# Kernel optimization log

Hardware: AMD Instinct MI355X
Metric: run time of the kernel (lower is better)

## Reference

```python
import jax, jax.numpy as jnp
import numpy as np

M_MARGIN = 0.5
SCALE = 64.0
COS_M = float(np.cos(M_MARGIN))
SIN_M = float(np.sin(M_MARGIN))
TH = -COS_M
MM = SIN_M * M_MARGIN
NUM_CLASSES = 100000
IN_FEATURES = 512
BATCH = 512


def setup_inputs() -> dict:
    key = jax.random.key(0)
    k1, k2, k3 = jax.random.split(key, 3)
    x = jax.random.normal(k1, (BATCH, IN_FEATURES), dtype=jnp.float32)
    y = jax.random.randint(k2, (BATCH,), 0, NUM_CLASSES, dtype=jnp.int64 if jax.config.jax_enable_x64 else jnp.int32)
    # xavier_uniform-like init for weight [num_classes, in_features]
    limit = float(np.sqrt(6.0 / (NUM_CLASSES + IN_FEATURES)))
    weight = jax.random.uniform(k3, (NUM_CLASSES, IN_FEATURES), minval=-limit, maxval=limit, dtype=jnp.float32)
    return {"x": x, "y": y, "weight": weight}


def _l2_normalize(v, axis=-1, eps=1e-12):
    # matches F.normalize(p=2): v / max(||v||, eps)
    n = jnp.sqrt(jnp.sum(v * v, axis=axis, keepdims=True))
    return v / jnp.maximum(n, eps)


def reference(x, y, weight):
    # cosine logits: [B, C]
    xn = _l2_normalize(x)
    wn = _l2_normalize(weight)
    cos = jnp.einsum('bd,cd->bc', xn, wn)
    sin = jnp.sqrt(jnp.clip(1.0 - cos * cos, 0.0))
    cos_w_margin = cos * COS_M - sin * SIN_M
    cos_w_margin = jnp.where(cos > TH, cos_w_margin, cos - MM)
    ohe = jax.nn.one_hot(y, NUM_CLASSES, dtype=jnp.bool_)
    logit = jnp.where(ohe, cos_w_margin, cos) * SCALE
    # cross entropy, mean reduction
    logp = jax.nn.log_softmax(logit, axis=-1)
    nll = -jnp.take_along_axis(logp, y[:, None], axis=-1)[:, 0]
    return jnp.mean(nll)
```

## Files before the change

kernel.cpp:

```cpp
#include <hip/hip_runtime.h>
#include <hip/hip_bf16.h>
#include <cstdint>
#include <cstddef>

#define C_CLS   100000
#define D_FEAT  512
#define B_ROWS  512
#define NBN     782
#define NBLK    (4 * NBN)

#define COSM 0.8775825618903728f
#define SINM 0.479425538604203f
#define TH_  (-0.8775825618903728f)
#define MM_  0.2397127693021015f

typedef __bf16 bf16x8 __attribute__((ext_vector_type(8)));
typedef float  f32x4  __attribute__((ext_vector_type(4)));

typedef __attribute__((address_space(3))) void lds_void;
typedef const __attribute__((address_space(1))) void g_void;

__device__ __forceinline__ void async_copy16(const void* g, void* l) {
    __builtin_amdgcn_global_load_lds((g_void*)g, (lds_void*)l, 16, 0, 0);
}

__global__ void k_norm(const float* __restrict__ x, const float* __restrict__ w,
                       __bf16* __restrict__ xn, __bf16* __restrict__ wn,
                       float* __restrict__ row_sum, int* __restrict__ counter) {
    const int r4   = blockIdx.x * 4 + (threadIdx.x >> 6);
    const int lane = threadIdx.x & 63;
    const float* src;
    __bf16*      dst;
    if (r4 < C_CLS) {
        src = w  + (size_t)r4 * D_FEAT;
        dst = wn + (size_t)r4 * D_FEAT;
    } else {
        src = x  + (size_t)(r4 - C_CLS) * D_FEAT;
        dst = xn + (size_t)(r4 - C_CLS) * D_FEAT;
    }
    const f32x4* p = (const f32x4*)src;
    f32x4 a = p[lane * 2];
    f32x4 b = p[lane * 2 + 1];
    float s = a[0]*a[0] + a[1]*a[1] + a[2]*a[2] + a[3]*a[3]
            + b[0]*b[0] + b[1]*b[1] + b[2]*b[2] + b[3]*b[3];
    #pragma unroll
    for (int m = 32; m >= 1; m >>= 1) s += __shfl_xor(s, m, 64);
    const float inv = 1.0f / fmaxf(sqrtf(s), 1e-12f);
    bf16x8 o;
    o[0] = (__bf16)(a[0]*inv); o[1] = (__bf16)(a[1]*inv);
    o[2] = (__bf16)(a[2]*inv); o[3] = (__bf16)(a[3]*inv);
    o[4] = (__bf16)(b[0]*inv); o[5] = (__bf16)(b[1]*inv);
    o[6] = (__bf16)(b[2]*inv); o[7] = (__bf16)(b[3]*inv);
    *(bf16x8*)(dst + lane * 8) = o;

    if (blockIdx.x == C_CLS / 4) {
        row_sum[threadIdx.x]       = 0.0f;
        row_sum[threadIdx.x + 256] = 0.0f;
        if (threadIdx.x == 0) *counter = 0;
    }
}

__global__ __launch_bounds__(256, 4) void k_gemm(
        const __bf16* __restrict__ xn, const __bf16* __restrict__ wn,
        const int* __restrict__ y,
        float* __restrict__ row_sum, float* __restrict__ tlogit,
        int* __restrict__ counter, float* __restrict__ out) {

    __shared__ __align__(16) __bf16 As[2][4096];
    __shared__ __align__(16) __bf16 Bs[2][4096];
    __shared__ int   ys[128];
    __shared__ float red[2][128];
    __shared__ int   lastflag;
    __shared__ float pr[4];

    const int tid = threadIdx.x;
    const int wg = (blockIdx.x & 7) * (NBLK / 8) + (blockIdx.x >> 3);
    const int bm = wg & 3;
    const int bn = wg >> 2;

    if (tid < 128) ys[tid] = y[bm * 128 + tid];

    const int wave = tid >> 6;
    const int lane = tid & 63;
    const int wm   = wave >> 1;
    const int wn_  = wave & 1;
    const int quad = lane >> 4;
    const int l15  = lane & 15;

    f32x4 acc[4][4];
    #pragma unroll
    for (int i = 0; i < 4; ++i)
        #pragma unroll
        for (int j = 0; j < 4; ++j) acc[i][j] = (f32x4){0.f, 0.f, 0.f, 0.f};

    #define STAGE(s, kt_) do {                                                          \
        const int k0_ = (kt_) * 32;                                                     \
        _Pragma("unroll")                                                               \
        for (int i_ = 0; i_ < 2; ++i_) {                                                \
            const int c_ = tid + i_ * 256;                                              \
            const int qc_ = c_ >> 7, rc_ = c_ & 127;                                    \
            async_copy16(xn + (size_t)(bm * 128 + rc_) * D_FEAT + k0_ + qc_ * 8,        \
                         &As[s][c_ * 8]);                                               \
        }                                                                               \
        _Pragma("unroll")                                                               \
        for (int i_ = 0; i_ < 2; ++i_) {                                                \
            const int c_ = tid + i_ * 256;                                              \
            const int qc_ = c_ >> 7, rc_ = c_ & 127;                                    \
            int grow_ = bn * 128 + rc_; if (grow_ > C_CLS - 1) grow_ = C_CLS - 1;       \
            async_copy16(wn + (size_t)grow_ * D_FEAT + k0_ + qc_ * 8,                   \
                         &Bs[s][c_ * 8]);                                               \
        }                                                                               \
    } while (0)

    STAGE(0, 0);
    STAGE(1, 1);

    #pragma unroll
    for (int kt = 0; kt < 16; ++kt) {
        const int cur = kt & 1;

        if (kt < 15) asm volatile("s_waitcnt vmcnt(4)" ::: "memory");
        else         asm volatile("s_waitcnt vmcnt(0)" ::: "memory");
        __builtin_amdgcn_s_barrier();

        bf16x8 af[4];
        #pragma unroll
        for (int mi = 0; mi < 4; ++mi)
            af[mi] = *(const bf16x8*)&As[cur][(quad * 128 + wm * 64 + mi * 16 + l15) * 8];
        bf16x8 bfr[4];
        #pragma unroll
        for (int ni = 0; ni < 4; ++ni)
            bfr[ni] = *(const bf16x8*)&Bs[cur][(quad * 128 + wn_ * 64 + ni * 16 + l15) * 8];

        asm volatile("s_waitcnt lgkmcnt(0)" ::: "memory");
        __builtin_amdgcn_s_barrier();
        if (kt < 14) STAGE(cur, kt + 2);

        #pragma unroll
        for (int mi = 0; mi < 4; ++mi)
            #pragma unroll
            for (int ni = 0; ni < 4; ++ni)
                acc[mi][ni] = __builtin_amdgcn_mfma_f32_16x16x32_bf16(af[mi], bfr[ni], acc[mi][ni], 0, 0, 0);
    }
    #undef STAGE

    #pragma unroll
    for (int mi = 0; mi < 4; ++mi) {
        float rs[4] = {0.f, 0.f, 0.f, 0.f};
        #pragma unroll
        for (int ni = 0; ni < 4; ++ni) {
            const int gcol = bn * 128 + wn_ * 64 + ni * 16 + l15;
            const bool colv = (gcol < C_CLS);
            #pragma unroll
            for (int reg = 0; reg < 4; ++reg) {
                const int lrow = wm * 64 + mi * 16 + quad * 4 + reg;
                const float cosv = acc[mi][ni][reg];
                const float sinv = sqrtf(fmaxf(1.0f - cosv * cosv, 0.0f));
                const float phi  = (cosv > TH_) ? (cosv * COSM - sinv * SINM) : (cosv - MM_);
                const bool ist   = colv && (gcol == ys[lrow]);
                const float logit = 64.0f * (ist ? phi : cosv);
                if (ist) atomicExch(&tlogit[bm * 128 + lrow], logit);
                rs[reg] += colv ? __expf(logit - 64.0f) : 0.0f;
            }
        }
        #pragma unroll
        for (int reg = 0; reg < 4; ++reg) {
            float v = rs[reg];
            v += __shfl_xor(v, 8, 64);
            v += __shfl_xor(v, 4, 64);
            v += __shfl_xor(v, 2, 64);
            v += __shfl_xor(v, 1, 64);
            if (l15 == 0) red[wn_][wm * 64 + mi * 16 + quad * 4 + reg] = v;
        }
    }
    __syncthreads();
    if (tid < 128) {
        const float v = red[0][tid] + red[1][tid];
        atomicAdd(&row_sum[bm * 128 + tid], v);
    }

    __syncthreads();
    if (tid == 0) {
        const int t = atomicAdd(counter, 1);
        lastflag = (t == NBLK - 1) ? 1 : 0;
    }
    __syncthreads();
    if (lastflag) {
        float part = 0.0f;
        #pragma unroll
        for (int i = 0; i < 2; ++i) {
            const int row = tid + i * 256;
            const float rsv = atomicAdd(&row_sum[row], 0.0f);
            const float tlv = atomicAdd(&tlogit[row], 0.0f);
            part += logf(rsv) + 64.0f - tlv;
        }
        #pragma unroll
        for (int m = 32; m >= 1; m >>= 1) part += __shfl_xor(part, m, 64);
        if ((tid & 63) == 0) pr[tid >> 6] = part;
        __syncthreads();
        if (tid == 0)
            out[0] = (pr[0] + pr[1] + pr[2] + pr[3]) * (1.0f / 512.0f);
    }
}

extern "C" void kernel_launch(void* const* d_in, const int* in_sizes, int n_in,
                              void* d_out, int out_size, void* d_ws, size_t ws_size,
                              hipStream_t stream) {
    const float* x = (const float*)d_in[0];
    const int*   y = (const int*)d_in[1];
    const float* w = (const float*)d_in[2];

    char* ws = (char*)d_ws;
    __bf16* xn      = (__bf16*)ws;
    __bf16* wn      = (__bf16*)(ws + 524288);
    float*  row_sum = (float*)(ws + 524288 + 102400000);
    float*  tlogit  = (float*)(ws + 524288 + 102400000 + 2048);
    int*    counter = (int*)(ws + 524288 + 102400000 + 4096);
    float*  out     = (float*)d_out;

    hipLaunchKernelGGL(k_norm, dim3((C_CLS + B_ROWS) / 4), dim3(256), 0, stream,
                       x, w, xn, wn, row_sum, counter);
    hipLaunchKernelGGL(k_gemm, dim3(NBLK), dim3(256), 0, stream,
                       xn, wn, y, row_sum, tlogit, counter, out);
}
```

Baseline: 415.6 us.

## Widen GEMM tile to 128x256 with 512 threads and triple-buffered K=64 stages

Doubles the class-dimension tile to 256 columns per block with 8 waves, raises the K step to 64, and replaces the double buffer with a 3-stage LDS ring so only one barrier is needed per iteration. It also adds s_setprio around the MFMA bursts and remaps blocks to XCDs with an uneven 196/195 split. The goal is to halve the number of blocks, improve reuse of the x tile, and cut barrier and LDS-read overhead. In exchange it uses far more LDS per block (about 144 KB), which lowers the number of blocks resident per CU.

```diff
diff --git a/kernel.cpp b/kernel.cpp
--- a/kernel.cpp
+++ b/kernel.cpp
@@ -6,7 +6,7 @@
 #define C_CLS   100000
 #define D_FEAT  512
 #define B_ROWS  512
-#define NBN     782
+#define NBN     391
 #define NBLK    (4 * NBN)
 
 #define COSM 0.8775825618903728f
@@ -60,30 +60,31 @@
     }
 }
 
-__global__ __launch_bounds__(256, 4) void k_gemm(
+__global__ __launch_bounds__(512, 2) void k_gemm(
         const __bf16* __restrict__ xn, const __bf16* __restrict__ wn,
         const int* __restrict__ y,
         float* __restrict__ row_sum, float* __restrict__ tlogit,
         int* __restrict__ counter, float* __restrict__ out) {
 
-    __shared__ __align__(16) __bf16 As[2][4096];
-    __shared__ __align__(16) __bf16 Bs[2][4096];
+    __shared__ __align__(16) __bf16 As[3][8192];
+    __shared__ __align__(16) __bf16 Bs[3][16384];
     __shared__ int   ys[128];
-    __shared__ float red[2][128];
+    __shared__ float red[4][128];
     __shared__ int   lastflag;
-    __shared__ float pr[4];
+    __shared__ float pr[8];
 
     const int tid = threadIdx.x;
-    const int wg = (blockIdx.x & 7) * (NBLK / 8) + (blockIdx.x >> 3);
-    const int bm = wg & 3;
-    const int bn = wg >> 2;
+    const int xcd = blockIdx.x & 7, o = blockIdx.x >> 3;
+    const int wg  = (xcd < 4 ? xcd * 196 : 784 + (xcd - 4) * 195) + o;
+    const int bm  = wg & 3;
+    const int bn  = wg >> 2;
 
     if (tid < 128) ys[tid] = y[bm * 128 + tid];
 
     const int wave = tid >> 6;
     const int lane = tid & 63;
-    const int wm   = wave >> 1;
-    const int wn_  = wave & 1;
+    const int wm   = wave >> 2;
+    const int wn_  = wave & 3;
     const int quad = lane >> 4;
     const int l15  = lane & 15;
 
@@ -94,20 +95,18 @@
         for (int j = 0; j < 4; ++j) acc[i][j] = (f32x4){0.f, 0.f, 0.f, 0.f};
 
     #define STAGE(s, kt_) do {                                                          \
-        const int k0_ = (kt_) * 32;                                                     \
+        const int k0_ = (kt_) * 64;                                                     \
         _Pragma("unroll")                                                               \
         for (int i_ = 0; i_ < 2; ++i_) {                                                \
-            const int c_ = tid + i_ * 256;                                              \
-            const int qc_ = c_ >> 7, rc_ = c_ & 127;                                    \
-            async_copy16(xn + (size_t)(bm * 128 + rc_) * D_FEAT + k0_ + qc_ * 8,        \
+            const int c_ = tid + i_ * 512;                                              \
+            async_copy16(xn + (size_t)(bm * 128 + (c_ & 127)) * D_FEAT + k0_ + (c_ >> 7) * 8, \
                          &As[s][c_ * 8]);                                               \
         }                                                                               \
         _Pragma("unroll")                                                               \
-        for (int i_ = 0; i_ < 2; ++i_) {                                                \
-            const int c_ = tid + i_ * 256;                                              \
-            const int qc_ = c_ >> 7, rc_ = c_ & 127;                                    \
-            int grow_ = bn * 128 + rc_; if (grow_ > C_CLS - 1) grow_ = C_CLS - 1;       \
-            async_copy16(wn + (size_t)grow_ * D_FEAT + k0_ + qc_ * 8,                   \
+        for (int i_ = 0; i_ < 4; ++i_) {                                                \
+            const int c_ = tid + i_ * 512;                                              \
+            int grow_ = bn * 256 + (c_ & 255); if (grow_ > C_CLS - 1) grow_ = C_CLS - 1; \
+            async_copy16(wn + (size_t)grow_ * D_FEAT + k0_ + (c_ >> 8) * 8,             \
                          &Bs[s][c_ * 8]);                                               \
         }                                                                               \
     } while (0)
@@ -116,31 +115,31 @@
     STAGE(1, 1);
 
     #pragma unroll
-    for (int kt = 0; kt < 16; ++kt) {
-        const int cur = kt & 1;
-
-        if (kt < 15) asm volatile("s_waitcnt vmcnt(4)" ::: "memory");
-        else         asm volatile("s_waitcnt vmcnt(0)" ::: "memory");
+    for (int t = 0; t < 8; ++t) {
+        const int cur = t % 3;
+
+        if (t < 7) asm volatile("s_waitcnt vmcnt(6)" ::: "memory");
+        else       asm volatile("s_waitcnt vmcnt(0)" ::: "memory");
         __builtin_amdgcn_s_barrier();
-
-        bf16x8 af[4];
-        #pragma unroll
-        for (int mi = 0; mi < 4; ++mi)
-            af[mi] = *(const bf16x8*)&As[cur][(quad * 128 + wm * 64 + mi * 16 + l15) * 8];
-        bf16x8 bfr[4];
-        #pragma unroll
-        for (int ni = 0; ni < 4; ++ni)
-            bfr[ni] = *(const bf16x8*)&Bs[cur][(quad * 128 + wn_ * 64 + ni * 16 + l15) * 8];
-
-        asm volatile("s_waitcnt lgkmcnt(0)" ::: "memory");
-        __builtin_amdgcn_s_barrier();
-        if (kt < 14) STAGE(cur, kt + 2);
-
-        #pragma unroll
-        for (int mi = 0; mi < 4; ++mi)
+        if (t < 6) STAGE((t + 2) % 3, t + 2);
+
+        #pragma unroll
+        for (int ks = 0; ks < 2; ++ks) {
+            bf16x8 af[4], bf[4];
+            #pragma unroll
+            for (int mi = 0; mi < 4; ++mi)
+                af[mi] = *(const bf16x8*)&As[cur][((ks * 4 + quad) * 128 + wm * 64 + mi * 16 + l15) * 8];
             #pragma unroll
             for (int ni = 0; ni < 4; ++ni)
-                acc[mi][ni] = __builtin_amdgcn_mfma_f32_16x16x32_bf16(af[mi], bfr[ni], acc[mi][ni], 0, 0, 0);
+                bf[ni] = *(const bf16x8*)&Bs[cur][((ks * 4 + quad) * 256 + wn_ * 64 + ni * 16 + l15) * 8];
+            __builtin_amdgcn_s_setprio(1);
+            #pragma unroll
+            for (int mi = 0; mi < 4; ++mi)
+                #pragma unroll
+                for (int ni = 0; ni < 4; ++ni)
+                    acc[mi][ni] = __builtin_amdgcn_mfma_f32_16x16x32_bf16(af[mi], bf[ni], acc[mi][ni], 0, 0, 0);
+            __builtin_amdgcn_s_setprio(0);
+        }
     }
     #undef STAGE
 
@@ -149,7 +148,7 @@
         float rs[4] = {0.f, 0.f, 0.f, 0.f};
         #pragma unroll
         for (int ni = 0; ni < 4; ++ni) {
-            const int gcol = bn * 128 + wn_ * 64 + ni * 16 + l15;
+            const int gcol = bn * 256 + wn_ * 64 + ni * 16 + l15;
             const bool colv = (gcol < C_CLS);
             #pragma unroll
             for (int reg = 0; reg < 4; ++reg) {
@@ -175,31 +174,30 @@
     }
     __syncthreads();
     if (tid < 128) {
-        const float v = red[0][tid] + red[1][tid];
+        const float v = red[0][tid] + red[1][tid] + red[2][tid] + red[3][tid];
         atomicAdd(&row_sum[bm * 128 + tid], v);
     }
 
     __syncthreads();
     if (tid == 0) {
-        const int t = atomicAdd(counter, 1);
-        lastflag = (t == NBLK - 1) ? 1 : 0;
+        const int tkt = atomicAdd(counter, 1);
+        lastflag = (tkt == NBLK - 1) ? 1 : 0;
     }
     __syncthreads();
     if (lastflag) {
-        float part = 0.0f;
-        #pragma unroll
-        for (int i = 0; i < 2; ++i) {
-            const int row = tid + i * 256;
-            const float rsv = atomicAdd(&row_sum[row], 0.0f);
-            const float tlv = atomicAdd(&tlogit[row], 0.0f);
-            part += logf(rsv) + 64.0f - tlv;
-        }
+        const float rsv = atomicAdd(&row_sum[tid], 0.0f);
+        const float tlv = atomicAdd(&tlogit[tid], 0.0f);
+        float part = logf(rsv) + 64.0f - tlv;
         #pragma unroll
         for (int m = 32; m >= 1; m >>= 1) part += __shfl_xor(part, m, 64);
         if ((tid & 63) == 0) pr[tid >> 6] = part;
         __syncthreads();
-        if (tid == 0)
-            out[0] = (pr[0] + pr[1] + pr[2] + pr[3]) * (1.0f / 512.0f);
+        if (tid == 0) {
+            float s = 0.0f;
+            #pragma unroll
+            for (int i = 0; i < 8; ++i) s += pr[i];
+            out[0] = s * (1.0f / 512.0f);
+        }
     }
 }
 
@@ -220,6 +218,6 @@
 
     hipLaunchKernelGGL(k_norm, dim3((C_CLS + B_ROWS) / 4), dim3(256), 0, stream,
                        x, w, xn, wn, row_sum, counter);
-    hipLaunchKernelGGL(k_gemm, dim3(NBLK), dim3(256), 0, stream,
+    hipLaunchKernelGGL(k_gemm, dim3(NBLK), dim3(512), 0, stream,
                        xn, wn, y, row_sum, tlogit, counter, out);
 }
```

Measured after the change: 489.7 us. +17.8%, slower.

## Load GEMM fragments directly from global memory instead of LDS staging

Applied to the files above, without the earlier changes.

Removes the double-buffered LDS staging via global_load_lds and has each wave load its MFMA A/B fragments straight from global memory (through L1/L2) per k-step. This drops the LDS footprint and per-iteration barriers, and relaxes launch bounds from 4 to 2 blocks per SM to allow more registers. In exchange, each fragment is fetched redundantly by the two waves that share it, accesses are strided 16-byte loads per row, and there is no explicit prefetch, so latency hiding depends on the compiler and on occupancy.

```diff
diff --git a/kernel.cpp b/kernel.cpp
--- a/kernel.cpp
+++ b/kernel.cpp
@@ -16,13 +16,6 @@
 
 typedef __bf16 bf16x8 __attribute__((ext_vector_type(8)));
 typedef float  f32x4  __attribute__((ext_vector_type(4)));
-
-typedef __attribute__((address_space(3))) void lds_void;
-typedef const __attribute__((address_space(1))) void g_void;
-
-__device__ __forceinline__ void async_copy16(const void* g, void* l) {
-    __builtin_amdgcn_global_load_lds((g_void*)g, (lds_void*)l, 16, 0, 0);
-}
 
 __global__ void k_norm(const float* __restrict__ x, const float* __restrict__ w,
                        __bf16* __restrict__ xn, __bf16* __restrict__ wn,
@@ -60,14 +53,12 @@
     }
 }
 
-__global__ __launch_bounds__(256, 4) void k_gemm(
+__global__ __launch_bounds__(256, 2) void k_gemm(
         const __bf16* __restrict__ xn, const __bf16* __restrict__ wn,
         const int* __restrict__ y,
         float* __restrict__ row_sum, float* __restrict__ tlogit,
         int* __restrict__ counter, float* __restrict__ out) {
 
-    __shared__ __align__(16) __bf16 As[2][4096];
-    __shared__ __align__(16) __bf16 Bs[2][4096];
     __shared__ int   ys[128];
     __shared__ float red[2][128];
     __shared__ int   lastflag;
@@ -87,62 +78,41 @@
     const int quad = lane >> 4;
     const int l15  = lane & 15;
 
+    const __bf16* aB[4];
+    #pragma unroll
+    for (int mi = 0; mi < 4; ++mi)
+        aB[mi] = xn + (size_t)(bm * 128 + wm * 64 + mi * 16 + l15) * D_FEAT + quad * 8;
+    const __bf16* bB[4];
+    #pragma unroll
+    for (int ni = 0; ni < 4; ++ni) {
+        int grow = bn * 128 + wn_ * 64 + ni * 16 + l15;
+        if (grow > C_CLS - 1) grow = C_CLS - 1;
+        bB[ni] = wn + (size_t)grow * D_FEAT + quad * 8;
+    }
+
     f32x4 acc[4][4];
     #pragma unroll
     for (int i = 0; i < 4; ++i)
         #pragma unroll
         for (int j = 0; j < 4; ++j) acc[i][j] = (f32x4){0.f, 0.f, 0.f, 0.f};
 
-    #define STAGE(s, kt_) do {                                                          \
-        const int k0_ = (kt_) * 32;                                                     \
-        _Pragma("unroll")                                                               \
-        for (int i_ = 0; i_ < 2; ++i_) {                                                \
-            const int c_ = tid + i_ * 256;                                              \
-            const int qc_ = c_ >> 7, rc_ = c_ & 127;                                    \
-            async_copy16(xn + (size_t)(bm * 128 + rc_) * D_FEAT + k0_ + qc_ * 8,        \
-                         &As[s][c_ * 8]);                                               \
-        }                                                                               \
-        _Pragma("unroll")                                                               \
-        for (int i_ = 0; i_ < 2; ++i_) {                                                \
-            const int c_ = tid + i_ * 256;                                              \
-            const int qc_ = c_ >> 7, rc_ = c_ & 127;                                    \
-            int grow_ = bn * 128 + rc_; if (grow_ > C_CLS - 1) grow_ = C_CLS - 1;       \
-            async_copy16(wn + (size_t)grow_ * D_FEAT + k0_ + qc_ * 8,                   \
-                         &Bs[s][c_ * 8]);                                               \
-        }                                                                               \
-    } while (0)
-
-    STAGE(0, 0);
-    STAGE(1, 1);
-
-    #pragma unroll
+    #pragma unroll 4
     for (int kt = 0; kt < 16; ++kt) {
-        const int cur = kt & 1;
-
-        if (kt < 15) asm volatile("s_waitcnt vmcnt(4)" ::: "memory");
-        else         asm volatile("s_waitcnt vmcnt(0)" ::: "memory");
-        __builtin_amdgcn_s_barrier();
-
-        bf16x8 af[4];
+        bf16x8 af[4], bfr[4];
         #pragma unroll
         for (int mi = 0; mi < 4; ++mi)
-            af[mi] = *(const bf16x8*)&As[cur][(quad * 128 + wm * 64 + mi * 16 + l15) * 8];
-        bf16x8 bfr[4];
+            af[mi] = *(const bf16x8*)(aB[mi] + kt * 32);
         #pragma unroll
         for (int ni = 0; ni < 4; ++ni)
-            bfr[ni] = *(const bf16x8*)&Bs[cur][(quad * 128 + wn_ * 64 + ni * 16 + l15) * 8];
-
-        asm volatile("s_waitcnt lgkmcnt(0)" ::: "memory");
-        __builtin_amdgcn_s_barrier();
-        if (kt < 14) STAGE(cur, kt + 2);
-
+            bfr[ni] = *(const bf16x8*)(bB[ni] + kt * 32);
         #pragma unroll
         for (int mi = 0; mi < 4; ++mi)
             #pragma unroll
             for (int ni = 0; ni < 4; ++ni)
                 acc[mi][ni] = __builtin_amdgcn_mfma_f32_16x16x32_bf16(af[mi], bfr[ni], acc[mi][ni], 0, 0, 0);
     }
-    #undef STAGE
+
+    __syncthreads();
 
     #pragma unroll
     for (int mi = 0; mi < 4; ++mi) {
```

Result: slower. 517.9 us (+24.6%).

## Fuse weight normalization into GEMM by loading fp32 weights and scaling after

Applied to the files above, without the earlier changes.

Removes the separate pass that normalized the weight matrix into a bf16 copy. The GEMM now streams fp32 weight tiles into LDS, converts them to bf16 in registers, and accumulates per-row sums of squares alongside. The accumulated cosine is then scaled by the inverse weight norm in the epilogue. This removes a full write and re-read of the bf16 weight copy, but doubles the weight bytes the GEMM loads, doubles LDS use for B (launch bounds lowered to 3 blocks per CU), and adds conversion work in the inner loop. Each weight tile is also re-read by the four blocks that share a column block, so those extra fp32 bytes are paid several times.

```diff
diff --git a/kernel.cpp b/kernel.cpp
--- a/kernel.cpp
+++ b/kernel.cpp
@@ -15,6 +15,7 @@
 #define MM_  0.2397127693021015f
 
 typedef __bf16 bf16x8 __attribute__((ext_vector_type(8)));
+typedef __bf16 bf16x4 __attribute__((ext_vector_type(4)));
 typedef float  f32x4  __attribute__((ext_vector_type(4)));
 
 typedef __attribute__((address_space(3))) void lds_void;
@@ -24,21 +25,11 @@
     __builtin_amdgcn_global_load_lds((g_void*)g, (lds_void*)l, 16, 0, 0);
 }
 
-__global__ void k_norm(const float* __restrict__ x, const float* __restrict__ w,
-                       __bf16* __restrict__ xn, __bf16* __restrict__ wn,
-                       float* __restrict__ row_sum, int* __restrict__ counter) {
-    const int r4   = blockIdx.x * 4 + (threadIdx.x >> 6);
+__global__ void k_xnorm(const float* __restrict__ x, __bf16* __restrict__ xn,
+                        float* __restrict__ row_sum, int* __restrict__ counter) {
+    const int row  = blockIdx.x * 4 + (threadIdx.x >> 6);
     const int lane = threadIdx.x & 63;
-    const float* src;
-    __bf16*      dst;
-    if (r4 < C_CLS) {
-        src = w  + (size_t)r4 * D_FEAT;
-        dst = wn + (size_t)r4 * D_FEAT;
-    } else {
-        src = x  + (size_t)(r4 - C_CLS) * D_FEAT;
-        dst = xn + (size_t)(r4 - C_CLS) * D_FEAT;
-    }
-    const f32x4* p = (const f32x4*)src;
+    const f32x4* p = (const f32x4*)(x + (size_t)row * D_FEAT);
     f32x4 a = p[lane * 2];
     f32x4 b = p[lane * 2 + 1];
     float s = a[0]*a[0] + a[1]*a[1] + a[2]*a[2] + a[3]*a[3]
@@ -51,23 +42,23 @@
     o[2] = (__bf16)(a[2]*inv); o[3] = (__bf16)(a[3]*inv);
     o[4] = (__bf16)(b[0]*inv); o[5] = (__bf16)(b[1]*inv);
     o[6] = (__bf16)(b[2]*inv); o[7] = (__bf16)(b[3]*inv);
-    *(bf16x8*)(dst + lane * 8) = o;
-
-    if (blockIdx.x == C_CLS / 4) {
+    *(bf16x8*)(xn + (size_t)row * D_FEAT + lane * 8) = o;
+
+    if (blockIdx.x == 0) {
         row_sum[threadIdx.x]       = 0.0f;
         row_sum[threadIdx.x + 256] = 0.0f;
         if (threadIdx.x == 0) *counter = 0;
     }
 }
 
-__global__ __launch_bounds__(256, 4) void k_gemm(
-        const __bf16* __restrict__ xn, const __bf16* __restrict__ wn,
+__global__ __launch_bounds__(256, 3) void k_gemm(
+        const __bf16* __restrict__ xn, const float* __restrict__ w,
         const int* __restrict__ y,
         float* __restrict__ row_sum, float* __restrict__ tlogit,
         int* __restrict__ counter, float* __restrict__ out) {
 
     __shared__ __align__(16) __bf16 As[2][4096];
-    __shared__ __align__(16) __bf16 Bs[2][4096];
+    __shared__ __align__(16) float  Bs[2][4096];
     __shared__ int   ys[128];
     __shared__ float red[2][128];
     __shared__ int   lastflag;
@@ -92,6 +83,7 @@
     for (int i = 0; i < 4; ++i)
         #pragma unroll
         for (int j = 0; j < 4; ++j) acc[i][j] = (f32x4){0.f, 0.f, 0.f, 0.f};
+    float ssq[4] = {0.f, 0.f, 0.f, 0.f};
 
     #define STAGE(s, kt_) do {                                                          \
         const int k0_ = (kt_) * 32;                                                     \
@@ -103,12 +95,12 @@
                          &As[s][c_ * 8]);                                               \
         }                                                                               \
         _Pragma("unroll")                                                               \
-        for (int i_ = 0; i_ < 2; ++i_) {                                                \
+        for (int i_ = 0; i_ < 4; ++i_) {                                                \
             const int c_ = tid + i_ * 256;                                              \
-            const int qc_ = c_ >> 7, rc_ = c_ & 127;                                    \
+            const int qc_ = c_ >> 8, hc_ = (c_ >> 7) & 1, rc_ = c_ & 127;               \
             int grow_ = bn * 128 + rc_; if (grow_ > C_CLS - 1) grow_ = C_CLS - 1;       \
-            async_copy16(wn + (size_t)grow_ * D_FEAT + k0_ + qc_ * 8,                   \
-                         &Bs[s][c_ * 8]);                                               \
+            async_copy16(w + (size_t)grow_ * D_FEAT + k0_ + qc_ * 8 + hc_ * 4,          \
+                         &Bs[s][c_ * 4]);                                               \
         }                                                                               \
     } while (0)
 
@@ -119,7 +111,7 @@
     for (int kt = 0; kt < 16; ++kt) {
         const int cur = kt & 1;
 
-        if (kt < 15) asm volatile("s_waitcnt vmcnt(4)" ::: "memory");
+        if (kt < 15) asm volatile("s_waitcnt vmcnt(6)" ::: "memory");
         else         asm volatile("s_waitcnt vmcnt(0)" ::: "memory");
         __builtin_amdgcn_s_barrier();
 
@@ -127,10 +119,20 @@
         #pragma unroll
         for (int mi = 0; mi < 4; ++mi)
             af[mi] = *(const bf16x8*)&As[cur][(quad * 128 + wm * 64 + mi * 16 + l15) * 8];
+
         bf16x8 bfr[4];
         #pragma unroll
-        for (int ni = 0; ni < 4; ++ni)
-            bfr[ni] = *(const bf16x8*)&Bs[cur][(quad * 128 + wn_ * 64 + ni * 16 + l15) * 8];
+        for (int ni = 0; ni < 4; ++ni) {
+            const int r = wn_ * 64 + ni * 16 + l15;
+            f32x4 b0 = *(const f32x4*)&Bs[cur][((quad * 2 + 0) * 128 + r) * 4];
+            f32x4 b1 = *(const f32x4*)&Bs[cur][((quad * 2 + 1) * 128 + r) * 4];
+            ssq[ni] += b0[0]*b0[0] + b0[1]*b0[1] + b0[2]*b0[2] + b0[3]*b0[3]
+                     + b1[0]*b1[0] + b1[1]*b1[1] + b1[2]*b1[2] + b1[3]*b1[3];
+            bf16x8 t;
+            t[0] = (__bf16)b0[0]; t[1] = (__bf16)b0[1]; t[2] = (__bf16)b0[2]; t[3] = (__bf16)b0[3];
+            t[4] = (__bf16)b1[0]; t[5] = (__bf16)b1[1]; t[6] = (__bf16)b1[2]; t[7] = (__bf16)b1[3];
+            bfr[ni] = t;
+        }
 
         asm volatile("s_waitcnt lgkmcnt(0)" ::: "memory");
         __builtin_amdgcn_s_barrier();
@@ -143,6 +145,15 @@
                 acc[mi][ni] = __builtin_amdgcn_mfma_f32_16x16x32_bf16(af[mi], bfr[ni], acc[mi][ni], 0, 0, 0);
     }
     #undef STAGE
+
+    float invw[4];
+    #pragma unroll
+    for (int ni = 0; ni < 4; ++ni) {
+        float s = ssq[ni];
+        s += __shfl_xor(s, 16, 64);
+        s += __shfl_xor(s, 32, 64);
+        invw[ni] = 1.0f / fmaxf(sqrtf(s), 1e-12f);
+    }
 
     #pragma unroll
     for (int mi = 0; mi < 4; ++mi) {
@@ -154,7 +165,7 @@
             #pragma unroll
             for (int reg = 0; reg < 4; ++reg) {
                 const int lrow = wm * 64 + mi * 16 + quad * 4 + reg;
-                const float cosv = acc[mi][ni][reg];
+                const float cosv = acc[mi][ni][reg] * invw[ni];
                 const float sinv = sqrtf(fmaxf(1.0f - cosv * cosv, 0.0f));
                 const float phi  = (cosv > TH_) ? (cosv * COSM - sinv * SINM) : (cosv - MM_);
                 const bool ist   = colv && (gcol == ys[lrow]);
@@ -212,14 +223,12 @@
 
     char* ws = (char*)d_ws;
     __bf16* xn      = (__bf16*)ws;
-    __bf16* wn      = (__bf16*)(ws + 524288);
-    float*  row_sum = (float*)(ws + 524288 + 102400000);
-    float*  tlogit  = (float*)(ws + 524288 + 102400000 + 2048);
-    int*    counter = (int*)(ws + 524288 + 102400000 + 4096);
+    float*  row_sum = (float*)(ws + 524288);
+    float*  tlogit  = (float*)(ws + 524288 + 2048);
+    int*    counter = (int*)(ws + 524288 + 4096);
     float*  out     = (float*)d_out;
 
-    hipLaunchKernelGGL(k_norm, dim3((C_CLS + B_ROWS) / 4), dim3(256), 0, stream,
-                       x, w, xn, wn, row_sum, counter);
+    hipLaunchKernelGGL(k_xnorm, dim3(128), dim3(256), 0, stream, x, xn, row_sum, counter);
     hipLaunchKernelGGL(k_gemm, dim3(NBLK), dim3(256), 0, stream,
-                       xn, wn, y, row_sum, tlogit, counter, out);
-}
+                       xn, w, y, row_sum, tlogit, counter, out);
+}
```

Result: slower. 428.2 us (+3.0%).
